# Kernel tuning notes

Hardware: AMD Instinct MI355X
Metric: run time of the kernel (lower is better)

The kernel has to match this reference:

```python
import jax, jax.numpy as jnp
import numpy as np

B, S, D = 2, 2048, 768
H = 12
HD = D // H


def setup_inputs() -> dict:
    key = jax.random.key(0)
    ks = jax.random.split(key, 9)
    s_in = 1.0 / np.sqrt(D)
    return {
        "x": jax.random.normal(ks[0], (B, S, D), dtype=jnp.float32),
        "wq": jax.random.normal(ks[1], (D, D), dtype=jnp.float32) * s_in,
        "bq": jax.random.normal(ks[2], (D,), dtype=jnp.float32) * 0.01,
        "wk": jax.random.normal(ks[3], (D, D), dtype=jnp.float32) * s_in,
        "bk": jax.random.normal(ks[4], (D,), dtype=jnp.float32) * 0.01,
        "wv": jax.random.normal(ks[5], (D, D), dtype=jnp.float32) * s_in,
        "bv": jax.random.normal(ks[6], (D,), dtype=jnp.float32) * 0.01,
        "wo": jax.random.normal(ks[7], (D, D), dtype=jnp.float32) * s_in,
        "bo": jax.random.normal(ks[8], (D,), dtype=jnp.float32) * 0.01,
    }


def reference(x, wq, bq, wk, bk, wv, bv, wo, bo):
    b, s, _ = x.shape
    # projections -> [b, h, s, hd]
    def proj(w, bias):
        return (x @ w + bias).reshape(b, s, H, HD).transpose(0, 2, 1, 3)
    q = proj(wq, bq)
    k = proj(wk, bk)
    v = proj(wv, bv)
    scores = jnp.einsum("bhqd,bhkd->bhqk", q, k)
    causal = jnp.triu(jnp.ones((s, s), dtype=bool), k=1)
    scores = jnp.where(causal, -jnp.inf, scores)
    attn = jax.nn.softmax(scores / np.sqrt(HD), axis=-1)
    # dropout p=0.0 -> identity
    ctx = jnp.einsum("bhqk,bhkd->bhqd", attn, v)
    ctx = ctx.transpose(0, 2, 1, 3).reshape(b, s, D)
    return ctx @ wo + bo
```

## Files before the change

kernel.cpp:

```cpp
#include <hip/hip_runtime.h>
#include <math.h>

#define BB  2
#define SS  2048
#define DD  768
#define HH  12
#define HDD 64
#define BSR (BB * SS)
#define NCH 40
#define NKT 12
#define NXB 1536

typedef __attribute__((ext_vector_type(8))) short bf16x8;
typedef __attribute__((ext_vector_type(4))) float f32x4;
typedef __attribute__((ext_vector_type(4))) int  i32x4;

__device__ inline f32x4 mfma16(bf16x8 a, bf16x8 b, f32x4 c) {
    return __builtin_amdgcn_mfma_f32_16x16x32_bf16(a, b, c, 0, 0, 0);
}

__device__ inline unsigned short f2b(float f) {
    unsigned int u = __float_as_uint(f);
    u += 0x7FFFu + ((u >> 16) & 1u);
    return (unsigned short)(u >> 16);
}
__device__ inline float b2f(unsigned short u) {
    return __uint_as_float((unsigned int)u << 16);
}

__device__ inline unsigned int cvt_pk_bf16(float lo, float hi) {
    unsigned int r;
    asm("v_cvt_pk_bf16_f32 %0, %1, %2" : "=v"(r) : "v"(lo), "v"(hi));
    return r;
}

__device__ inline void async_copy16(void* lds, const void* g) {
    __builtin_amdgcn_global_load_lds(
        (const __attribute__((address_space(1))) unsigned int*)g,
        (__attribute__((address_space(3))) unsigned int*)lds, 16, 0, 0);
}

__global__ __launch_bounds__(256) void conv_all_kernel(
    const float* __restrict__ x,
    const float* __restrict__ w0, const float* __restrict__ w1,
    const float* __restrict__ w2, const float* __restrict__ w3,
    unsigned short* __restrict__ xb,
    unsigned short* __restrict__ o0, unsigned short* __restrict__ o1,
    unsigned short* __restrict__ o2, unsigned short* __restrict__ o3)
{
    const int blk = blockIdx.x;
    const int tid = threadIdx.x;

    __shared__ unsigned short tile[64][72];

    if (blk < NXB) {
        const size_t i = ((size_t)blk * 256 + tid) * 8;
        float4 f0 = *(const float4*)&x[i];
        float4 f1 = *(const float4*)&x[i + 4];
        i32x4 tv;
        tv[0] = (int)cvt_pk_bf16(f0.x, f0.y);
        tv[1] = (int)cvt_pk_bf16(f0.z, f0.w);
        tv[2] = (int)cvt_pk_bf16(f1.x, f1.y);
        tv[3] = (int)cvt_pk_bf16(f1.z, f1.w);
        *(i32x4*)&xb[i] = tv;
    } else {
        const int b2  = blk - NXB;
        const int z   = b2 / 144;
        const int idx = b2 % 144;
        const int n0  = (idx % 12) * 64;
        const int k0  = (idx / 12) * 64;
        const float* w = (z == 0) ? w0 : (z == 1) ? w1 : (z == 2) ? w2 : w3;
        unsigned short* o = (z == 0) ? o0 : (z == 1) ? o1 : (z == 2) ? o2 : o3;

#pragma unroll
        for (int p = 0; p < 4; ++p) {
            int c  = p * 256 + tid;
            int kr = c >> 4;
            int nc = (c & 15) * 4;
            float4 v = *(const float4*)&w[(size_t)(k0 + kr) * DD + n0 + nc];
            tile[nc + 0][kr] = f2b(v.x);
            tile[nc + 1][kr] = f2b(v.y);
            tile[nc + 2][kr] = f2b(v.z);
            tile[nc + 3][kr] = f2b(v.w);
        }
        __syncthreads();
#pragma unroll
        for (int p = 0; p < 2; ++p) {
            int c  = p * 256 + tid;
            int nr = c >> 3;
            int kc = (c & 7) * 8;
            *(i32x4*)&o[(size_t)(n0 + nr) * DD + k0 + kc] = *(const i32x4*)&tile[nr][kc];
        }
    }
}

__global__ __launch_bounds__(256) void qkv_gemm_kernel(
    const unsigned short* __restrict__ xb,
    const unsigned short* __restrict__ wqT, const unsigned short* __restrict__ wkT,
    const unsigned short* __restrict__ wvT,
    const float* __restrict__ bq, const float* __restrict__ bk,
    const float* __restrict__ bv,
    unsigned short* __restrict__ Qg, unsigned short* __restrict__ Kg,
    unsigned short* __restrict__ Vg)
{
    const int p0   = blockIdx.x;
    const int xcd  = p0 & 7;
    const int slot = p0 >> 3;
    const int m_t  = (slot / 18) * 8 + xcd;
    const int nw   = slot % 18;
    const int n_t  = nw / 3;
    const int which = nw % 3;

    const unsigned short* Bt = (which == 0) ? wqT : (which == 1) ? wkT : wvT;
    const float* bias        = (which == 0) ? bq  : (which == 1) ? bk  : bv;
    unsigned short* out      = (which == 0) ? Qg  : (which == 1) ? Kg  : Vg;
    const float qs           = (which == 0) ? 0.18033688011112042f : 1.0f;

    const int m0 = m_t * 64;
    const int n0 = n_t * 128;
    const int tid  = threadIdx.x;
    const int w    = tid >> 6;
    const int lane = tid & 63;
    const int quad = lane >> 4;
    const int l16  = lane & 15;
    const int mh   = w & 1;
    const int nh   = w >> 1;
    const int swz  = l16 & 7;

    __shared__ unsigned short smem[24576];
    unsigned short (*As0)[64] = (unsigned short(*)[64])smem;
    unsigned short (*Bs0)[64] = (unsigned short(*)[64])(smem + 4096);
    unsigned short (*As1)[64] = (unsigned short(*)[64])(smem + 12288);
    unsigned short (*Bs1)[64] = (unsigned short(*)[64])(smem + 16384);
    unsigned short (*T)[136]  = (unsigned short(*)[136])smem;

    const unsigned short* gA[2];
    int ldsA[2];
#pragma unroll
    for (int p = 0; p < 2; ++p) {
        int c  = p * 256 + tid;
        int r  = c >> 3;
        int j  = c & 7;
        int ch = j ^ (r & 7);
        gA[p]   = &xb[(size_t)(m0 + r) * DD + ch * 8];
        ldsA[p] = r * 64 + j * 8;
    }
    const unsigned short* gB[4];
    int ldsB[4];
#pragma unroll
    for (int p = 0; p < 4; ++p) {
        int c  = p * 256 + tid;
        int r  = c >> 3;
        int j  = c & 7;
        int ch = j ^ (r & 7);
        gB[p]   = &Bt[(size_t)(n0 + r) * DD + ch * 8];
        ldsB[p] = r * 64 + j * 8;
    }

    f32x4 zero = {0.f, 0.f, 0.f, 0.f};
    f32x4 acc[2][4];
#pragma unroll
    for (int i = 0; i < 2; ++i)
#pragma unroll
        for (int j = 0; j < 4; ++j) acc[i][j] = zero;

#pragma unroll
    for (int p = 0; p < 2; ++p) async_copy16((unsigned short*)As0 + ldsA[p], gA[p]);
#pragma unroll
    for (int p = 0; p < 4; ++p) async_copy16((unsigned short*)Bs0 + ldsB[p], gB[p]);
    __syncthreads();

#pragma unroll
    for (int t = 0; t < NKT; ++t) {
        const int kn = (t + 1) * 64;
        unsigned short (*As)[64] = (t & 1) ? As1 : As0;
        unsigned short (*Bs)[64] = (t & 1) ? Bs1 : Bs0;
        unsigned short (*An)[64] = (t & 1) ? As0 : As1;
        unsigned short (*Bn)[64] = (t & 1) ? Bs0 : Bs1;
        if (t + 1 < NKT) {
#pragma unroll
            for (int p = 0; p < 2; ++p)
                async_copy16((unsigned short*)An + ldsA[p], gA[p] + kn);
#pragma unroll
            for (int p = 0; p < 4; ++p)
                async_copy16((unsigned short*)Bn + ldsB[p], gB[p] + kn);
        }
        bf16x8 af0[2], af1[2], bf0[4], bf1[4];
#pragma unroll
        for (int mt = 0; mt < 2; ++mt) {
            int r = mh * 32 + mt * 16 + l16;
            af0[mt] = *(const bf16x8*)&As[r][((quad    ) ^ swz) * 8];
            af1[mt] = *(const bf16x8*)&As[r][((quad + 4) ^ swz) * 8];
        }
#pragma unroll
        for (int nt = 0; nt < 4; ++nt) {
            int r = nh * 64 + nt * 16 + l16;
            bf0[nt] = *(const bf16x8*)&Bs[r][((quad    ) ^ swz) * 8];
            bf1[nt] = *(const bf16x8*)&Bs[r][((quad + 4) ^ swz) * 8];
        }
#pragma unroll
        for (int mt = 0; mt < 2; ++mt)
#pragma unroll
            for (int nt = 0; nt < 4; ++nt) {
                acc[mt][nt] = mfma16(af0[mt], bf0[nt], acc[mt][nt]);
                acc[mt][nt] = mfma16(af1[mt], bf1[nt], acc[mt][nt]);
            }
        __syncthreads();
    }

    if (which < 2) {
#pragma unroll
        for (int nt = 0; nt < 4; ++nt) {
            const int col = nh * 64 + nt * 16 + l16;
            const float bvv = bias[n0 + col];
#pragma unroll
            for (int mt = 0; mt < 2; ++mt)
#pragma unroll
                for (int r = 0; r < 4; ++r)
                    T[mh * 32 + mt * 16 + quad * 4 + r][col] =
                        f2b((acc[mt][nt][r] + bvv) * qs);
        }
        __syncthreads();
#pragma unroll
        for (int p2 = 0; p2 < 4; ++p2) {
            int c    = p2 * 256 + tid;
            int row  = c >> 4;
            int ck   = c & 15;
            int head = ck >> 3;
            int wi   = ck & 7;
            int sg   = m0 + row;
            int bi   = sg >> 11, si = sg & 2047;
            int hcol = (n0 >> 6) + head;
            *(i32x4*)&out[(((size_t)(bi * HH + hcol)) * SS + si) * HDD + wi * 8] =
                *(const i32x4*)&T[row][head * 64 + wi * 8];
        }
    } else {
        for (int pass = 0; pass < 2; ++pass) {
            if (pass) __syncthreads();
            if (nh == pass) {
#pragma unroll
                for (int nt = 0; nt < 4; ++nt) {
                    const float bvv = bias[n0 + pass * 64 + nt * 16 + l16];
#pragma unroll
                    for (int mt = 0; mt < 2; ++mt) {
                        uint2 pk;
                        pk.x = cvt_pk_bf16(acc[mt][nt][0] + bvv, acc[mt][nt][1] + bvv);
                        pk.y = cvt_pk_bf16(acc[mt][nt][2] + bvv, acc[mt][nt][3] + bvv);
                        *(uint2*)&T[nt * 16 + l16][mh * 32 + mt * 16 + quad * 4] = pk;
                    }
                }
            }
            __syncthreads();
            const int bi   = m0 >> 11;
            const int s0   = m0 & 2047;
            const int hcol = (n0 >> 6) + pass;
#pragma unroll
            for (int p2 = 0; p2 < 2; ++p2) {
                int c    = p2 * 256 + tid;
                int drow = c >> 3;
                int wi   = c & 7;
                *(i32x4*)&out[(((size_t)(bi * HH + hcol)) * HDD + drow) * SS + s0 + wi * 8] =
                    *(const i32x4*)&T[drow][wi * 8];
            }
        }
    }
}

__global__ __launch_bounds__(256) void out_gemm_kernel(
    const unsigned short* __restrict__ cb, const unsigned short* __restrict__ woT,
    const float* __restrict__ bo, float* __restrict__ out)
{
    const int p0   = blockIdx.x;
    const int xcd  = p0 & 7;
    const int slot = p0 >> 3;
    const int m0 = ((slot / 6) * 8 + xcd) * 64;
    const int n0 = (slot % 6) * 128;
    const int tid  = threadIdx.x;
    const int w    = tid >> 6;
    const int lane = tid & 63;
    const int quad = lane >> 4;
    const int l16  = lane & 15;
    const int mh   = w & 1;
    const int nh   = w >> 1;
    const int swz  = l16 & 7;

    __shared__ unsigned short smem[24576];
    unsigned short (*As0)[64] = (unsigned short(*)[64])smem;
    unsigned short (*Bs0)[64] = (unsigned short(*)[64])(smem + 4096);
    unsigned short (*As1)[64] = (unsigned short(*)[64])(smem + 12288);
    unsigned short (*Bs1)[64] = (unsigned short(*)[64])(smem + 16384);

    const unsigned short* gA[2];
    int ldsA[2];
#pragma unroll
    for (int p = 0; p < 2; ++p) {
        int c  = p * 256 + tid;
        int r  = c >> 3;
        int j  = c & 7;
        int ch = j ^ (r & 7);
        gA[p]   = &cb[(size_t)(m0 + r) * DD + ch * 8];
        ldsA[p] = r * 64 + j * 8;
    }
    const unsigned short* gB[4];
    int ldsB[4];
#pragma unroll
    for (int p = 0; p < 4; ++p) {
        int c  = p * 256 + tid;
        int r  = c >> 3;
        int j  = c & 7;
        int ch = j ^ (r & 7);
        gB[p]   = &woT[(size_t)(n0 + r) * DD + ch * 8];
        ldsB[p] = r * 64 + j * 8;
    }

    f32x4 zero = {0.f, 0.f, 0.f, 0.f};
    f32x4 acc[2][4];
#pragma unroll
    for (int i = 0; i < 2; ++i)
#pragma unroll
        for (int j = 0; j < 4; ++j) acc[i][j] = zero;

#pragma unroll
    for (int p = 0; p < 2; ++p) async_copy16((unsigned short*)As0 + ldsA[p], gA[p]);
#pragma unroll
    for (int p = 0; p < 4; ++p) async_copy16((unsigned short*)Bs0 + ldsB[p], gB[p]);
    __syncthreads();

#pragma unroll
    for (int t = 0; t < NKT; ++t) {
        const int kn = (t + 1) * 64;
        unsigned short (*As)[64] = (t & 1) ? As1 : As0;
        unsigned short (*Bs)[64] = (t & 1) ? Bs1 : Bs0;
        unsigned short (*An)[64] = (t & 1) ? As0 : As1;
        unsigned short (*Bn)[64] = (t & 1) ? Bs0 : Bs1;
        if (t + 1 < NKT) {
#pragma unroll
            for (int p = 0; p < 2; ++p)
                async_copy16((unsigned short*)An + ldsA[p], gA[p] + kn);
#pragma unroll
            for (int p = 0; p < 4; ++p)
                async_copy16((unsigned short*)Bn + ldsB[p], gB[p] + kn);
        }
        bf16x8 af0[2], af1[2], bf0[4], bf1[4];
#pragma unroll
        for (int mt = 0; mt < 2; ++mt) {
            int r = mh * 32 + mt * 16 + l16;
            af0[mt] = *(const bf16x8*)&As[r][((quad    ) ^ swz) * 8];
            af1[mt] = *(const bf16x8*)&As[r][((quad + 4) ^ swz) * 8];
        }
#pragma unroll
        for (int nt = 0; nt < 4; ++nt) {
            int r = nh * 64 + nt * 16 + l16;
            bf0[nt] = *(const bf16x8*)&Bs[r][((quad    ) ^ swz) * 8];
            bf1[nt] = *(const bf16x8*)&Bs[r][((quad + 4) ^ swz) * 8];
        }
#pragma unroll
        for (int mt = 0; mt < 2; ++mt)
#pragma unroll
            for (int nt = 0; nt < 4; ++nt) {
                acc[mt][nt] = mfma16(af0[mt], bf0[nt], acc[mt][nt]);
                acc[mt][nt] = mfma16(af1[mt], bf1[nt], acc[mt][nt]);
            }
        __syncthreads();
    }

#pragma unroll
    for (int nt = 0; nt < 4; ++nt) {
        const int n = n0 + nh * 64 + nt * 16 + l16;
        const float bvv = bo[n];
#pragma unroll
        for (int mt = 0; mt < 2; ++mt) {
            const int mbase = m0 + mh * 32 + mt * 16 + quad * 4;
#pragma unroll
            for (int r = 0; r < 4; ++r)
                out[(size_t)(mbase + r) * DD + n] = acc[mt][nt][r] + bvv;
        }
    }
}

__global__ __launch_bounds__(256, 4) void attn_mfma_kernel(
    const unsigned short* __restrict__ Qg, const unsigned short* __restrict__ Kg,
    const unsigned short* __restrict__ Vg, unsigned short* __restrict__ Opart,
    float* __restrict__ Lb)
{
    const int p0   = blockIdx.x;
    const int xcd  = p0 & 7;
    const int slot = p0 >> 3;
    const int bh_i = (slot / 40) * 8 + xcd;
    const int c    = (NCH - 1) - (slot % 40);

    int qt, ck, nch;
    if (c < 4)       { qt = c;                            ck = 0;     nch = 1; }
    else if (c < 12) { int t = c - 4;  qt = 4  + (t >> 1); ck = t & 1; nch = 2; }
    else if (c < 24) { int t = c - 12; qt = 8  + t / 3;    ck = t % 3; nch = 3; }
    else             { int t = c - 24; qt = 12 + (t >> 2); ck = t & 3; nch = 4; }
    const int NT   = 2 * qt + 2;
    const int base = NT / nch, rem = NT % nch;
    const int lo   = ck * base + min(ck, rem);
    const int hi   = lo + base + (ck < rem ? 1 : 0);
    const int dlo  = 2 * qt;

    const int tid  = threadIdx.x;
    const int w    = tid >> 6;
    const int lane = tid & 63;
    const int quad = lane >> 4;
    const int l16  = lane & 15;
    const int q0   = qt * 128;

    const size_t bh = (size_t)bh_i;
    const unsigned short* qp = Qg + bh * SS * HDD;
    const unsigned short* kp = Kg + bh * SS * HDD;
    const unsigned short* vp = Vg + bh * HDD * SS;

    unsigned short* op = Opart + ((size_t)bh * NCH + c) * 128 * HDD;
    float* lp = Lb + ((size_t)bh * NCH + c) * 128;

    __shared__ unsigned short Ks[64][64];
    __shared__ unsigned short Vt[64][64];
    __shared__ unsigned short PsT[4][2][16][72];
    unsigned short* slab = &PsT[w][0][0][0];

    bf16x8 qb0[2], qb1[2];
    int query[2];
#pragma unroll
    for (int qf = 0; qf < 2; ++qf) {
        query[qf] = q0 + w * 32 + qf * 16 + l16;
        qb0[qf] = *(const bf16x8*)&qp[(size_t)query[qf] * HDD + quad * 8];
        qb1[qf] = *(const bf16x8*)&qp[(size_t)query[qf] * HDD + 32 + quad * 8];
    }

    const int pr  = tid >> 3;
    const int po8 = tid & 7;
    const int fs  = l16 & 7;

    i32x4 kpre[2], vpre[2];
#pragma unroll
    for (int p = 0; p < 2; ++p) {
        int r  = pr + p * 32;
        int gc = (po8 ^ (r & 7)) * 8;
        kpre[p] = *(const i32x4*)&kp[(size_t)(lo * 64 + r) * HDD + gc];
        vpre[p] = *(const i32x4*)&vp[(size_t)r * SS + lo * 64 + gc];
    }

    f32x4 zero = {0.f, 0.f, 0.f, 0.f};
    f32x4 o_acc[2][4];
    float l_i[2] = {0.f, 0.f};
#pragma unroll
    for (int qf = 0; qf < 2; ++qf)
#pragma unroll
        for (int i = 0; i < 4; ++i) o_acc[qf][i] = zero;

    for (int kt = lo; kt < hi; ++kt) {
        const int k0 = kt * 64;
        __syncthreads();
#pragma unroll
        for (int p = 0; p < 2; ++p) {
            int r = pr + p * 32;
            *(i32x4*)&Ks[r][po8 * 8] = kpre[p];
            *(i32x4*)&Vt[r][po8 * 8] = vpre[p];
        }
        __syncthreads();

        if (kt + 1 < hi) {
            const int kn = (kt + 1) * 64;
#pragma unroll
            for (int p = 0; p < 2; ++p) {
                int r  = pr + p * 32;
                int gc = (po8 ^ (r & 7)) * 8;
                kpre[p] = *(const i32x4*)&kp[(size_t)(kn + r) * HDD + gc];
                vpre[p] = *(const i32x4*)&vp[(size_t)r * SS + kn + gc];
            }
        }

        const bool diag = (kt >= dlo);
#pragma unroll
        for (int t = 0; t < 4; ++t) {
            const int row = t * 16 + l16;
            bf16x8 klo = *(const bf16x8*)&Ks[row][((quad    ) ^ fs) * 8];
            bf16x8 khi = *(const bf16x8*)&Ks[row][((quad + 4) ^ fs) * 8];
#pragma unroll
            for (int qf = 0; qf < 2; ++qf) {
                f32x4 s = mfma16(klo, qb0[qf], zero);
                s = mfma16(khi, qb1[qf], s);
                float pv[4];
#pragma unroll
                for (int r = 0; r < 4; ++r) {
                    const int key = k0 + t * 16 + quad * 4 + r;
                    float p = exp2f(s[r]);
                    if (diag && key > query[qf]) p = 0.f;
                    pv[r] = p;
                    l_i[qf] += p;
                }
                uint2 pk;
                pk.x = cvt_pk_bf16(pv[0], pv[1]);
                pk.y = cvt_pk_bf16(pv[2], pv[3]);
                *(uint2*)&slab[(qf * 16 + l16) * 72 + t * 16 + quad * 4] = pk;
            }
        }

        bf16x8 pb0[2], pb1[2];
#pragma unroll
        for (int qf = 0; qf < 2; ++qf) {
            pb0[qf] = *(const bf16x8*)&slab[(qf * 16 + l16) * 72 + quad * 8];
            pb1[qf] = *(const bf16x8*)&slab[(qf * 16 + l16) * 72 + 32 + quad * 8];
        }
#pragma unroll
        for (int t2 = 0; t2 < 4; ++t2) {
            const int row = t2 * 16 + l16;
            bf16x8 vlo = *(const bf16x8*)&Vt[row][((quad    ) ^ fs) * 8];
            bf16x8 vhi = *(const bf16x8*)&Vt[row][((quad + 4) ^ fs) * 8];
#pragma unroll
            for (int qf = 0; qf < 2; ++qf) {
                o_acc[qf][t2] = mfma16(vlo, pb0[qf], o_acc[qf][t2]);
                o_acc[qf][t2] = mfma16(vhi, pb1[qf], o_acc[qf][t2]);
            }
        }
    }

#pragma unroll
    for (int qf = 0; qf < 2; ++qf) {
        float l = l_i[qf];
        l += __shfl_xor(l, 16);
        l += __shfl_xor(l, 32);
        if (quad == 0) lp[w * 32 + qf * 16 + l16] = l;
#pragma unroll
        for (int t2 = 0; t2 < 4; ++t2) {
            uint2 pk;
            pk.x = cvt_pk_bf16(o_acc[qf][t2][0], o_acc[qf][t2][1]);
            pk.y = cvt_pk_bf16(o_acc[qf][t2][2], o_acc[qf][t2][3]);
            *(uint2*)&slab[(qf * 16 + l16) * 72 + t2 * 16 + quad * 4] = pk;
        }
    }
#pragma unroll
    for (int p2 = 0; p2 < 4; ++p2) {
        int cc  = p2 * 64 + lane;
        int row = cc >> 3, dc = cc & 7;
        *(i32x4*)&op[(size_t)(w * 32 + row) * HDD + dc * 8] =
            *(const i32x4*)&slab[row * 72 + dc * 8];
    }
}

__global__ __launch_bounds__(256) void merge_kernel(
    const unsigned short* __restrict__ Opart, const float* __restrict__ Lb,
    unsigned short* __restrict__ cb)
{
    const int bx   = blockIdx.x;
    const int qt2  = bx >> 1;
    const int half = bx & 1;
    const int bhn  = blockIdx.y;
    const int b    = bhn / HH, h = bhn % HH;
    const int tid  = threadIdx.x;
    const int row  = tid >> 2;
    const int d0   = (tid & 3) * 16;
    const int rowc = half * 64 + row;
    const int q    = qt2 * 128 + rowc;

    const int nch = (qt2 < 4) ? 1 : (qt2 < 8) ? 2 : (qt2 < 12) ? 3 : 4;
    const int cb0 = (qt2 < 4) ? qt2
                  : (qt2 < 8)  ? (4  + (qt2 - 4)  * 2)
                  : (qt2 < 12) ? (12 + (qt2 - 8)  * 3)
                  :              (24 + (qt2 - 12) * 4);

    float suml = 0.f;
    float accv[16];
#pragma unroll
    for (int i = 0; i < 16; ++i) accv[i] = 0.f;

    for (int ci = 0; ci < nch; ++ci) {
        const size_t base = (size_t)bhn * NCH + cb0 + ci;
        suml += Lb[base * 128 + rowc];
        const unsigned short* o = Opart + (base * 128 + rowc) * HDD + d0;
        i32x4 va = *(const i32x4*)&o[0];
        i32x4 vb = *(const i32x4*)&o[8];
#pragma unroll
        for (int wd = 0; wd < 4; ++wd) {
            unsigned int ua = (unsigned int)va[wd];
            accv[wd * 2 + 0] += __uint_as_float(ua << 16);
            accv[wd * 2 + 1] += __uint_as_float(ua & 0xffff0000u);
            unsigned int ub = (unsigned int)vb[wd];
            accv[8 + wd * 2 + 0] += __uint_as_float(ub << 16);
            accv[8 + wd * 2 + 1] += __uint_as_float(ub & 0xffff0000u);
        }
    }
    const float inv = 1.0f / suml;
    unsigned int res[8];
#pragma unroll
    for (int i = 0; i < 8; ++i)
        res[i] = cvt_pk_bf16(accv[2 * i] * inv, accv[2 * i + 1] * inv);
    unsigned short* dst = &cb[((size_t)(b * SS + q)) * DD + h * HDD + d0];
    *(i32x4*)&dst[0] = *(const i32x4*)&res[0];
    *(i32x4*)&dst[8] = *(const i32x4*)&res[4];
}

extern "C" void kernel_launch(void* const* d_in, const int* in_sizes, int n_in,
                              void* d_out, int out_size, void* d_ws, size_t ws_size,
                              hipStream_t stream)
{
    const float* x  = (const float*)d_in[0];
    const float* wq = (const float*)d_in[1];
    const float* bq = (const float*)d_in[2];
    const float* wk = (const float*)d_in[3];
    const float* bk = (const float*)d_in[4];
    const float* wv = (const float*)d_in[5];
    const float* bv = (const float*)d_in[6];
    const float* wo = (const float*)d_in[7];
    const float* bo = (const float*)d_in[8];
    float* out = (float*)d_out;

    char* p = (char*)d_ws;
    const size_t XB  = (size_t)BSR * DD * 2;
    const size_t WB  = (size_t)DD * DD * 2;
    const size_t OPB = (size_t)BB * HH * NCH * 128 * HDD * 2;
    const size_t LBB = (size_t)BB * HH * NCH * 128 * 4;
    unsigned short* wqT = (unsigned short*)p;            p += WB;
    unsigned short* wkT = (unsigned short*)p;            p += WB;
    unsigned short* wvT = (unsigned short*)p;            p += WB;
    unsigned short* woT = (unsigned short*)p;            p += WB;
    unsigned short* xb  = (unsigned short*)p;            p += XB;
    unsigned short* Qg  = (unsigned short*)p;            p += XB;
    unsigned short* Kg  = (unsigned short*)p;            p += XB;
    unsigned short* Vg  = (unsigned short*)p;            p += XB;
    unsigned short* cb  = (unsigned short*)p;            p += XB;
    unsigned short* Opart = (unsigned short*)p;          p += OPB;
    float* Lb = (float*)p;                               p += LBB;

    conv_all_kernel<<<dim3(NXB + 576), 256, 0, stream>>>(
        x, wq, wk, wv, wo, xb, wqT, wkT, wvT, woT);
    qkv_gemm_kernel<<<dim3(1152), 256, 0, stream>>>(
        xb, wqT, wkT, wvT, bq, bk, bv, Qg, Kg, Vg);
    attn_mfma_kernel<<<dim3(960), 256, 0, stream>>>(
        Qg, Kg, Vg, Opart, Lb);
    merge_kernel<<<dim3(32, BB * HH), 256, 0, stream>>>(Opart, Lb, cb);
    out_gemm_kernel<<<dim3(384), 256, 0, stream>>>(cb, woT, bo, out);
}
```

Before: 150.6 us.

## Normalize single-chunk attention tiles in-kernel, raise MFMA priority, split diagonal masking path

Query tiles covered by a single key chunk now normalize their output by 1/l inside the attention kernel and write straight into the context buffer. The merge kernel then handles only the multi-chunk tiles, so its grid shrinks. The softmax loop gets a branch that skips the causal mask compare on tiles off the diagonal, and the MFMA sections are wrapped in s_setprio to favour matrix issue across waves. This adds branching and a second output path to the attention epilogue.

```diff
diff --git a/kernel.cpp b/kernel.cpp
--- a/kernel.cpp
+++ b/kernel.cpp
@@ -381,7 +381,7 @@
 __global__ __launch_bounds__(256, 4) void attn_mfma_kernel(
     const unsigned short* __restrict__ Qg, const unsigned short* __restrict__ Kg,
     const unsigned short* __restrict__ Vg, unsigned short* __restrict__ Opart,
-    float* __restrict__ Lb)
+    float* __restrict__ Lb, unsigned short* __restrict__ cbg)
 {
     const int p0   = blockIdx.x;
     const int xcd  = p0 & 7;
@@ -480,16 +480,26 @@
             bf16x8 khi = *(const bf16x8*)&Ks[row][((quad + 4) ^ fs) * 8];
 #pragma unroll
             for (int qf = 0; qf < 2; ++qf) {
+                __builtin_amdgcn_s_setprio(1);
                 f32x4 s = mfma16(klo, qb0[qf], zero);
                 s = mfma16(khi, qb1[qf], s);
+                __builtin_amdgcn_s_setprio(0);
                 float pv[4];
-#pragma unroll
-                for (int r = 0; r < 4; ++r) {
-                    const int key = k0 + t * 16 + quad * 4 + r;
-                    float p = exp2f(s[r]);
-                    if (diag && key > query[qf]) p = 0.f;
-                    pv[r] = p;
-                    l_i[qf] += p;
+                if (!diag) {
+#pragma unroll
+                    for (int r = 0; r < 4; ++r) {
+                        pv[r] = exp2f(s[r]);
+                        l_i[qf] += pv[r];
+                    }
+                } else {
+#pragma unroll
+                    for (int r = 0; r < 4; ++r) {
+                        const int key = k0 + t * 16 + quad * 4 + r;
+                        float p = exp2f(s[r]);
+                        if (key > query[qf]) p = 0.f;
+                        pv[r] = p;
+                        l_i[qf] += p;
+                    }
                 }
                 uint2 pk;
                 pk.x = cvt_pk_bf16(pv[0], pv[1]);
@@ -504,6 +514,7 @@
             pb0[qf] = *(const bf16x8*)&slab[(qf * 16 + l16) * 72 + quad * 8];
             pb1[qf] = *(const bf16x8*)&slab[(qf * 16 + l16) * 72 + 32 + quad * 8];
         }
+        __builtin_amdgcn_s_setprio(1);
 #pragma unroll
         for (int t2 = 0; t2 < 4; ++t2) {
             const int row = t2 * 16 + l16;
@@ -515,6 +526,7 @@
                 o_acc[qf][t2] = mfma16(vhi, pb1[qf], o_acc[qf][t2]);
             }
         }
+        __builtin_amdgcn_s_setprio(0);
     }
 
 #pragma unroll
@@ -522,21 +534,44 @@
         float l = l_i[qf];
         l += __shfl_xor(l, 16);
         l += __shfl_xor(l, 32);
-        if (quad == 0) lp[w * 32 + qf * 16 + l16] = l;
-#pragma unroll
-        for (int t2 = 0; t2 < 4; ++t2) {
-            uint2 pk;
-            pk.x = cvt_pk_bf16(o_acc[qf][t2][0], o_acc[qf][t2][1]);
-            pk.y = cvt_pk_bf16(o_acc[qf][t2][2], o_acc[qf][t2][3]);
-            *(uint2*)&slab[(qf * 16 + l16) * 72 + t2 * 16 + quad * 4] = pk;
-        }
-    }
-#pragma unroll
-    for (int p2 = 0; p2 < 4; ++p2) {
-        int cc  = p2 * 64 + lane;
-        int row = cc >> 3, dc = cc & 7;
-        *(i32x4*)&op[(size_t)(w * 32 + row) * HDD + dc * 8] =
-            *(const i32x4*)&slab[row * 72 + dc * 8];
+        if (nch == 1) {
+            const float inv = 1.0f / l;
+#pragma unroll
+            for (int t2 = 0; t2 < 4; ++t2) {
+                uint2 pk;
+                pk.x = cvt_pk_bf16(o_acc[qf][t2][0] * inv, o_acc[qf][t2][1] * inv);
+                pk.y = cvt_pk_bf16(o_acc[qf][t2][2] * inv, o_acc[qf][t2][3] * inv);
+                *(uint2*)&slab[(qf * 16 + l16) * 72 + t2 * 16 + quad * 4] = pk;
+            }
+        } else {
+            if (quad == 0) lp[w * 32 + qf * 16 + l16] = l;
+#pragma unroll
+            for (int t2 = 0; t2 < 4; ++t2) {
+                uint2 pk;
+                pk.x = cvt_pk_bf16(o_acc[qf][t2][0], o_acc[qf][t2][1]);
+                pk.y = cvt_pk_bf16(o_acc[qf][t2][2], o_acc[qf][t2][3]);
+                *(uint2*)&slab[(qf * 16 + l16) * 72 + t2 * 16 + quad * 4] = pk;
+            }
+        }
+    }
+    if (nch == 1) {
+        const int b = bh_i / HH, h = bh_i % HH;
+#pragma unroll
+        for (int p2 = 0; p2 < 4; ++p2) {
+            int cc  = p2 * 64 + lane;
+            int row = cc >> 3, dc = cc & 7;
+            const int q = q0 + w * 32 + row;
+            *(i32x4*)&cbg[((size_t)(b * SS + q)) * DD + h * HDD + dc * 8] =
+                *(const i32x4*)&slab[row * 72 + dc * 8];
+        }
+    } else {
+#pragma unroll
+        for (int p2 = 0; p2 < 4; ++p2) {
+            int cc  = p2 * 64 + lane;
+            int row = cc >> 3, dc = cc & 7;
+            *(i32x4*)&op[(size_t)(w * 32 + row) * HDD + dc * 8] =
+                *(const i32x4*)&slab[row * 72 + dc * 8];
+        }
     }
 }
 
@@ -545,7 +580,7 @@
     unsigned short* __restrict__ cb)
 {
     const int bx   = blockIdx.x;
-    const int qt2  = bx >> 1;
+    const int qt2  = 4 + (bx >> 1);
     const int half = bx & 1;
     const int bhn  = blockIdx.y;
     const int b    = bhn / HH, h = bhn % HH;
@@ -555,9 +590,8 @@
     const int rowc = half * 64 + row;
     const int q    = qt2 * 128 + rowc;
 
-    const int nch = (qt2 < 4) ? 1 : (qt2 < 8) ? 2 : (qt2 < 12) ? 3 : 4;
-    const int cb0 = (qt2 < 4) ? qt2
-                  : (qt2 < 8)  ? (4  + (qt2 - 4)  * 2)
+    const int nch = (qt2 < 8) ? 2 : (qt2 < 12) ? 3 : 4;
+    const int cb0 = (qt2 < 8)  ? (4  + (qt2 - 4)  * 2)
                   : (qt2 < 12) ? (12 + (qt2 - 8)  * 3)
                   :              (24 + (qt2 - 12) * 4);
 
@@ -629,7 +663,7 @@
     qkv_gemm_kernel<<<dim3(1152), 256, 0, stream>>>(
         xb, wqT, wkT, wvT, bq, bk, bv, Qg, Kg, Vg);
     attn_mfma_kernel<<<dim3(960), 256, 0, stream>>>(
-        Qg, Kg, Vg, Opart, Lb);
-    merge_kernel<<<dim3(32, BB * HH), 256, 0, stream>>>(Opart, Lb, cb);
+        Qg, Kg, Vg, Opart, Lb, cb);
+    merge_kernel<<<dim3(24, BB * HH), 256, 0, stream>>>(Opart, Lb, cb);
     out_gemm_kernel<<<dim3(384), 256, 0, stream>>>(cb, woT, bo, out);
 }
```

After: 150.7 us. No clear change (+0.1%).
